# Kernel tuning notes

Hardware: AMD Instinct MI355X
Metric: run time of the kernel (lower is better)

Reference implementation:

```python
import jax, jax.numpy as jnp
import numpy as np

B, NAG = 8192, 16          # scenes, agents per scene
CIN, CH = 64, 128          # gnn_in_channels, gnn_out_channels
R2 = 8.0 * 8.0             # comm_range squared
BOX = 20.0                 # positions sampled uniformly in [0, BOX]^2


def _lin(k, fi, fo):
    k1, k2 = jax.random.split(k)
    s = 1.0 / np.sqrt(fi)
    W = jax.random.uniform(k1, (fi, fo), jnp.float32, -s, s)
    b = jax.random.uniform(k2, (fo,), jnp.float32, -s, s)
    return W, b


def setup_inputs() -> dict:
    key = jax.random.key(0)
    ks = jax.random.split(key, 10)
    x = jax.random.normal(ks[0], (B * NAG, CIN), jnp.float32)          # VAE mu per agent
    pos = jax.random.uniform(ks[1], (B, NAG, 2), jnp.float32) * BOX    # sensor xy positions
    W_rel1, b_rel1 = _lin(ks[2], CIN, CH)
    W_root1, _ = _lin(ks[3], CIN, CH)
    W_rel2, b_rel2 = _lin(ks[4], CH, CH)
    W_root2, _ = _lin(ks[5], CH, CH)
    Wh1, bh1 = _lin(ks[6], 2 * CH, 64)
    Wh2, bh2 = _lin(ks[7], 64, 32)
    Wh3, bh3 = _lin(ks[8], 32, 16)
    return dict(x=x, pos=pos, W_rel1=W_rel1, b_rel1=b_rel1, W_root1=W_root1,
                W_rel2=W_rel2, b_rel2=b_rel2, W_root2=W_root2,
                Wh1=Wh1, bh1=bh1, Wh2=Wh2, bh2=bh2, Wh3=Wh3, bh3=bh3)


def _graph_conv(h, adj, W_rel, b_rel, W_root):
    # PyG GraphConv (aggr='add'): out_i = W_rel @ sum_{j in N(i)} h_j + b_rel + W_root @ h_i
    nb = adj.shape[0]
    hb = h.reshape(nb, NAG, h.shape[-1])                 # [B, n, C]
    agg = jnp.einsum('bij,bjc->bic', adj, hb)            # neighbor sum within each scene
    return agg.reshape(h.shape[0], -1) @ W_rel + b_rel + h @ W_root


def reference(x, pos, W_rel1, b_rel1, W_root1, W_rel2, b_rel2, W_root2,
              Wh1, bh1, Wh2, bh2, Wh3, bh3):
    # radius_graph (batch-isolated, loop=False) as a per-scene dense mask
    diff = pos[:, :, None, :] - pos[:, None, :, :]       # [B, n, n, 2]
    d2 = jnp.sum(diff * diff, axis=-1)                   # [B, n, n]
    eye = jnp.eye(NAG, dtype=bool)
    adj = ((d2 <= R2) & ~eye).astype(x.dtype)            # [B, n, n]
    # Dropout(p=0.2) omitted (eval / deterministic reference).
    x1 = jax.nn.relu(_graph_conv(x, adj, W_rel1, b_rel1, W_root1))   # named 'x1' (inplace ReLU)
    x2 = jax.nn.relu(_graph_conv(x1, adj, W_rel2, b_rel2, W_root2))  # named 'x2' (inplace ReLU)
    h = jnp.concatenate([x1, x2], axis=-1)               # JumpingKnowledge('cat')
    h = jax.nn.relu(h @ Wh1 + bh1)
    h = jax.nn.relu(h @ Wh2 + bh2)
    out = h @ Wh3 + bh3                                  # [N, 16]
    return out.reshape(B, NAG, 16)
```

## Files before the change

kernel.cpp:

```cpp
#include <hip/hip_runtime.h>

#define NAG 16
#define SPB 4
#define NBLK 2048
#define R2f 64.0f

typedef unsigned short u16;
typedef __attribute__((ext_vector_type(8))) short short8;
typedef __attribute__((ext_vector_type(4))) float f32x4;

#define MFMA(a, b, c) __builtin_amdgcn_mfma_f32_16x16x32_bf16(a, b, c, 0, 0, 0)

#define OFF_B1 0
#define OFF_B2 16384
#define OFF_H1 49152
#define OFF_H2 65536
#define OFF_H3 67584
#define SWZ_UNITS 8512

__device__ __forceinline__ u16 f2b(float f) {
    unsigned u = __float_as_uint(f);
    unsigned r = u + 0x7FFFu + ((u >> 16) & 1u);
    return (u16)(r >> 16);
}
__device__ __forceinline__ unsigned rb(float f) {
    return (__float_as_uint(f) + 0x8000u) >> 16;
}
__device__ __forceinline__ unsigned pk2(float a, float b) {
    return ((__float_as_uint(a) + 0x8000u) >> 16) |
           ((__float_as_uint(b) + 0x8000u) & 0xFFFF0000u);
}

__global__ __launch_bounds__(256) void swizzle_w(
    const float* __restrict__ Wrel1, const float* __restrict__ Wroot1,
    const float* __restrict__ Wrel2, const float* __restrict__ Wroot2,
    const float* __restrict__ Wh1,  const float* __restrict__ Wh2,
    const float* __restrict__ Wh3,  u16* __restrict__ ws)
{
    const int u = blockIdx.x * 256 + threadIdx.x;
    if (u >= SWZ_UNITS) return;
    int v, T, N, ksplit;
    const float *W, *W2;
    u16* dst;
    if (u < 2048)      { v = u;        T = 8; N = 128; ksplit = 64;  W = Wroot1; W2 = Wrel1; dst = ws + OFF_B1 + v * 8; }
    else if (u < 6144) { v = u - 2048; T = 8; N = 128; ksplit = 128; W = Wroot2; W2 = Wrel2; dst = ws + OFF_B2 + v * 8; }
    else if (u < 8192) { v = u - 6144; T = 4; N = 64;  ksplit = 1 << 30; W = Wh1; W2 = Wh1; dst = ws + OFF_H1 + v * 8; }
    else if (u < 8448) { v = u - 8192; T = 2; N = 32;  ksplit = 1 << 30; W = Wh2; W2 = Wh2; dst = ws + OFF_H2 + v * 8; }
    else               { v = u - 8448; T = 1; N = 16;  ksplit = 1 << 30; W = Wh3; W2 = Wh3; dst = ws + OFF_H3 + v * 8; }
    const int lane = v & 63;
    const int t = (v >> 6) % T;
    const int s = (v >> 6) / T;
    const int n = t * 16 + (lane & 15);
    const int k0 = s * 32 + (lane >> 4) * 8;
    #pragma unroll
    for (int j = 0; j < 8; ++j) {
        const int k = k0 + j;
        const float val = (k < ksplit) ? W[k * N + n] : W2[(k - ksplit) * N + n];
        dst[j] = f2b(val);
    }
}

__device__ __forceinline__ short8 ldfrag(const u16* __restrict__ ws, int off,
                                         int T, int s, int tile, int lane) {
    return *(const short8*)(ws + off + (size_t)(((s * T + tile) * 64 + lane) * 8));
}

__device__ __forceinline__ short8 make_adjA(unsigned m, int q, int odd) {
    union { short8 v; unsigned u[4]; } r;
    const bool on = (q >> 1) == odd;
    const int base = (q & 1) * 8;
    #pragma unroll
    for (int jj = 0; jj < 4; ++jj) {
        const int k0 = base + 2 * jj;
        const unsigned lo = (on && ((m >> k0) & 1u)) ? 0x3F80u : 0u;
        const unsigned hi = (on && ((m >> (k0 + 1)) & 1u)) ? 0x3F80u : 0u;
        r.u[jj] = lo | (hi << 16);
    }
    return r.v;
}

__global__ __launch_bounds__(256) void gnn_fused5(
    const float* __restrict__ x, const float* __restrict__ pos,
    const float* __restrict__ brel1, const float* __restrict__ brel2,
    const float* __restrict__ bh1,  const float* __restrict__ bh2,
    const float* __restrict__ bh3,
    const u16* __restrict__ ws, float* __restrict__ out)
{
    __shared__ __align__(16) u16 pool[26624];
    __shared__ unsigned mask[64];
    u16* const xb  = pool;
    u16* const yT  = pool + 8704;
    u16* const x1b = pool + 17920;

    const int t = threadIdx.x;
    const int wv = t >> 6, lane = t & 63, ln = lane & 15, q = lane >> 4;
    const int c0 = 32 * wv;
    const int n0 = 2 * wv, n1 = 2 * wv + 1;
    const size_t sA = (size_t)blockIdx.x * SPB;

    {
        const int r = t >> 2, co = (t & 3) * 16;
        const float* src = x + (sA * 16 + r) * 64 + co;
        const float4 v0 = *(const float4*)(src);
        const float4 v1 = *(const float4*)(src + 4);
        const float4 v2 = *(const float4*)(src + 8);
        const float4 v3 = *(const float4*)(src + 12);
        uint4 ua, ub;
        ua.x = pk2(v0.x, v0.y); ua.y = pk2(v0.z, v0.w);
        ua.z = pk2(v1.x, v1.y); ua.w = pk2(v1.z, v1.w);
        ub.x = pk2(v2.x, v2.y); ub.y = pk2(v2.z, v2.w);
        ub.z = pk2(v3.x, v3.y); ub.w = pk2(v3.z, v3.w);
        *(uint4*)&xb[r * 136 + co]     = ua;
        *(uint4*)&xb[r * 136 + co + 8] = ub;
    }
    if (t < 64) {
        const int g = t >> 4, a = t & 15;
        const float* pp = pos + (sA + g) * (NAG * 2);
        const float ax = pp[2 * a], ay = pp[2 * a + 1];
        unsigned m = 0;
        for (int j = 0; j < NAG; ++j) {
            const float dx = ax - pp[2 * j], dy = ay - pp[2 * j + 1];
            if (dx * dx + dy * dy <= R2f && j != a) m |= (1u << j);
        }
        mask[g * 16 + a] = m;
    }
    __syncthreads();

    short8 adjA[4];
    #pragma unroll
    for (int g = 0; g < 4; ++g) adjA[g] = make_adjA(mask[g * 16 + ln], q, g & 1);

    {
        short8 Brl[2][2], Bro[2][2], Af[4][2];
        #pragma unroll
        for (int s = 0; s < 2; ++s) {
            Brl[s][0] = ldfrag(ws, OFF_B1, 8, s + 2, n0, lane);
            Brl[s][1] = ldfrag(ws, OFF_B1, 8, s + 2, n1, lane);
        }
        #pragma unroll
        for (int m = 0; m < 4; ++m) {
            Af[m][0] = *(const short8*)&xb[(m * 16 + ln) * 136 + q * 8];
            Af[m][1] = *(const short8*)&xb[(m * 16 + ln) * 136 + 32 + q * 8];
            f32x4 a0 = {0.f, 0.f, 0.f, 0.f}, a1 = a0;
            a0 = MFMA(Af[m][0], Brl[0][0], a0); a0 = MFMA(Af[m][1], Brl[1][0], a0);
            a1 = MFMA(Af[m][0], Brl[0][1], a1); a1 = MFMA(Af[m][1], Brl[1][1], a1);
            uint2 u0; u0.x = pk2(a0[0], a0[1]); u0.y = pk2(a0[2], a0[3]);
            uint2 u1; u1.x = pk2(a1[0], a1[1]); u1.y = pk2(a1[2], a1[3]);
            *(uint2*)&yT[(c0 + ln) * 72 + m * 16 + q * 4]      = u0;
            *(uint2*)&yT[(c0 + 16 + ln) * 72 + m * 16 + q * 4] = u1;
        }
        short8 By[2][2];
        #pragma unroll
        for (int w = 0; w < 2; ++w) {
            By[w][0] = *(const short8*)&yT[(c0 + ln) * 72 + w * 32 + q * 8];
            By[w][1] = *(const short8*)&yT[(c0 + 16 + ln) * 72 + w * 32 + q * 8];
        }
        #pragma unroll
        for (int s = 0; s < 2; ++s) {
            Bro[s][0] = ldfrag(ws, OFF_B1, 8, s, n0, lane);
            Bro[s][1] = ldfrag(ws, OFF_B1, 8, s, n1, lane);
        }
        const float b0 = brel1[c0 + ln], b1 = brel1[c0 + 16 + ln];
        #pragma unroll
        for (int g = 0; g < 4; ++g) {
            f32x4 a0 = {b0, b0, b0, b0}, a1 = {b1, b1, b1, b1};
            a0 = MFMA(Af[g][0], Bro[0][0], a0); a0 = MFMA(Af[g][1], Bro[1][0], a0);
            a1 = MFMA(Af[g][0], Bro[0][1], a1); a1 = MFMA(Af[g][1], Bro[1][1], a1);
            a0 = MFMA(adjA[g], By[g >> 1][0], a0);
            a1 = MFMA(adjA[g], By[g >> 1][1], a1);
            #pragma unroll
            for (int r = 0; r < 4; ++r) {
                const int row = g * 16 + q * 4 + r;
                x1b[row * 136 + c0 + ln]      = (u16)rb(fmaxf(a0[r], 0.f));
                x1b[row * 136 + c0 + 16 + ln] = (u16)rb(fmaxf(a1[r], 0.f));
            }
        }
    }
    __syncthreads();

    {
        short8 Brl[4][2];
        #pragma unroll
        for (int s = 0; s < 4; ++s) {
            Brl[s][0] = ldfrag(ws, OFF_B2, 8, s + 4, n0, lane);
            Brl[s][1] = ldfrag(ws, OFF_B2, 8, s + 4, n1, lane);
        }
        #pragma unroll
        for (int m = 0; m < 4; ++m) {
            f32x4 a0 = {0.f, 0.f, 0.f, 0.f}, a1 = a0;
            #pragma unroll
            for (int s = 0; s < 4; ++s) {
                const short8 A = *(const short8*)&x1b[(m * 16 + ln) * 136 + s * 32 + q * 8];
                a0 = MFMA(A, Brl[s][0], a0);
                a1 = MFMA(A, Brl[s][1], a1);
            }
            uint2 u0; u0.x = pk2(a0[0], a0[1]); u0.y = pk2(a0[2], a0[3]);
            uint2 u1; u1.x = pk2(a1[0], a1[1]); u1.y = pk2(a1[2], a1[3]);
            *(uint2*)&yT[(c0 + ln) * 72 + m * 16 + q * 4]      = u0;
            *(uint2*)&yT[(c0 + 16 + ln) * 72 + m * 16 + q * 4] = u1;
        }
        short8 By[2][2];
        #pragma unroll
        for (int w = 0; w < 2; ++w) {
            By[w][0] = *(const short8*)&yT[(c0 + ln) * 72 + w * 32 + q * 8];
            By[w][1] = *(const short8*)&yT[(c0 + 16 + ln) * 72 + w * 32 + q * 8];
        }
        short8 Bro[4][2];
        #pragma unroll
        for (int s = 0; s < 4; ++s) {
            Bro[s][0] = ldfrag(ws, OFF_B2, 8, s, n0, lane);
            Bro[s][1] = ldfrag(ws, OFF_B2, 8, s, n1, lane);
        }
        const float b0 = brel2[c0 + ln], b1 = brel2[c0 + 16 + ln];
        #pragma unroll
        for (int g = 0; g < 4; ++g) {
            f32x4 a0 = {b0, b0, b0, b0}, a1 = {b1, b1, b1, b1};
            #pragma unroll
            for (int s = 0; s < 4; ++s) {
                const short8 A = *(const short8*)&x1b[(g * 16 + ln) * 136 + s * 32 + q * 8];
                a0 = MFMA(A, Bro[s][0], a0);
                a1 = MFMA(A, Bro[s][1], a1);
            }
            a0 = MFMA(adjA[g], By[g >> 1][0], a0);
            a1 = MFMA(adjA[g], By[g >> 1][1], a1);
            #pragma unroll
            for (int r = 0; r < 4; ++r) {
                const int row = g * 16 + q * 4 + r;
                xb[row * 136 + c0 + ln]      = (u16)rb(fmaxf(a0[r], 0.f));
                xb[row * 136 + c0 + 16 + ln] = (u16)rb(fmaxf(a1[r], 0.f));
            }
        }
    }
    __syncthreads();

    {
        short8 Bf[8];
        #pragma unroll
        for (int s = 0; s < 8; ++s) Bf[s] = ldfrag(ws, OFF_H1, 4, s, wv, lane);
        const float b = bh1[wv * 16 + ln];
        #pragma unroll
        for (int m = 0; m < 4; ++m) {
            f32x4 a = {b, b, b, b}, c = {0.f, 0.f, 0.f, 0.f};
            #pragma unroll
            for (int s = 0; s < 4; ++s) {
                const short8 A1 = *(const short8*)&x1b[(m * 16 + ln) * 136 + s * 32 + q * 8];
                const short8 A2 = *(const short8*)&xb[(m * 16 + ln) * 136 + s * 32 + q * 8];
                a = MFMA(A1, Bf[s], a);
                c = MFMA(A2, Bf[s + 4], c);
            }
            #pragma unroll
            for (int r = 0; r < 4; ++r)
                yT[(m * 16 + q * 4 + r) * 72 + wv * 16 + ln] = (u16)rb(fmaxf(a[r] + c[r], 0.f));
        }
    }
    __syncthreads();

    {
        const u16* h1b = yT;
        u16* h2b = x1b;
        const short8 A0 = *(const short8*)&h1b[(wv * 16 + ln) * 72 + q * 8];
        const short8 A1 = *(const short8*)&h1b[(wv * 16 + ln) * 72 + 32 + q * 8];
        #pragma unroll
        for (int nt = 0; nt < 2; ++nt) {
            const short8 B0 = ldfrag(ws, OFF_H2, 2, 0, nt, lane);
            const short8 B1 = ldfrag(ws, OFF_H2, 2, 1, nt, lane);
            const float b = bh2[nt * 16 + ln];
            f32x4 a = {b, b, b, b};
            a = MFMA(A0, B0, a);
            a = MFMA(A1, B1, a);
            #pragma unroll
            for (int r = 0; r < 4; ++r)
                h2b[(wv * 16 + q * 4 + r) * 40 + nt * 16 + ln] = (u16)rb(fmaxf(a[r], 0.f));
        }
        const short8 A = *(const short8*)&h2b[(wv * 16 + ln) * 40 + q * 8];
        const short8 B = ldfrag(ws, OFF_H3, 1, 0, 0, lane);
        const float b = bh3[ln];
        f32x4 a = {b, b, b, b};
        a = MFMA(A, B, a);
        #pragma unroll
        for (int r = 0; r < 4; ++r)
            out[(sA * 16 + wv * 16 + q * 4 + r) * 16 + ln] = a[r];
    }
}

extern "C" void kernel_launch(void* const* d_in, const int* in_sizes, int n_in,
                              void* d_out, int out_size, void* d_ws, size_t ws_size,
                              hipStream_t stream) {
    const float* x      = (const float*)d_in[0];
    const float* pos    = (const float*)d_in[1];
    const float* Wrel1  = (const float*)d_in[2];
    const float* brel1  = (const float*)d_in[3];
    const float* Wroot1 = (const float*)d_in[4];
    const float* Wrel2  = (const float*)d_in[5];
    const float* brel2  = (const float*)d_in[6];
    const float* Wroot2 = (const float*)d_in[7];
    const float* Wh1    = (const float*)d_in[8];
    const float* bh1    = (const float*)d_in[9];
    const float* Wh2    = (const float*)d_in[10];
    const float* bh2    = (const float*)d_in[11];
    const float* Wh3    = (const float*)d_in[12];
    const float* bh3    = (const float*)d_in[13];
    u16* ws = (u16*)d_ws;

    swizzle_w<<<(SWZ_UNITS + 255) / 256, 256, 0, stream>>>(
        Wrel1, Wroot1, Wrel2, Wroot2, Wh1, Wh2, Wh3, ws);
    gnn_fused5<<<NBLK, 256, 0, stream>>>(
        x, pos, brel1, brel2, bh1, bh2, bh3, ws, (float*)d_out);
}
```

Measured before the change: 125.0 us.

## Double block to 512 threads, one 16-column tile per wave

Each block now has eight waves instead of four. In the GraphConv layers each wave owns one 16-column output tile rather than two. The first head layer splits work by column tile and row half, and the final head layers run on four waves only. The aim is more wavefronts and more latency hiding per CU with fewer registers per wave. The cost is that each A-fragment read from LDS is now repeated across more waves, and the idle waves in the tail stage waste slots.

```diff
diff --git a/kernel.cpp b/kernel.cpp
--- a/kernel.cpp
+++ b/kernel.cpp
@@ -3,6 +3,7 @@
 #define NAG 16
 #define SPB 4
 #define NBLK 2048
+#define TPB 512
 #define R2f 64.0f
 
 typedef unsigned short u16;
@@ -79,7 +80,7 @@
     return r.v;
 }
 
-__global__ __launch_bounds__(256) void gnn_fused5(
+__global__ __launch_bounds__(TPB) void gnn_fused6(
     const float* __restrict__ x, const float* __restrict__ pos,
     const float* __restrict__ brel1, const float* __restrict__ brel2,
     const float* __restrict__ bh1,  const float* __restrict__ bh2,
@@ -94,24 +95,18 @@
 
     const int t = threadIdx.x;
     const int wv = t >> 6, lane = t & 63, ln = lane & 15, q = lane >> 4;
-    const int c0 = 32 * wv;
-    const int n0 = 2 * wv, n1 = 2 * wv + 1;
+    const int c0 = 16 * wv;
     const size_t sA = (size_t)blockIdx.x * SPB;
 
     {
-        const int r = t >> 2, co = (t & 3) * 16;
+        const int r = t >> 3, co = (t & 7) * 8;
         const float* src = x + (sA * 16 + r) * 64 + co;
         const float4 v0 = *(const float4*)(src);
         const float4 v1 = *(const float4*)(src + 4);
-        const float4 v2 = *(const float4*)(src + 8);
-        const float4 v3 = *(const float4*)(src + 12);
-        uint4 ua, ub;
+        uint4 ua;
         ua.x = pk2(v0.x, v0.y); ua.y = pk2(v0.z, v0.w);
         ua.z = pk2(v1.x, v1.y); ua.w = pk2(v1.z, v1.w);
-        ub.x = pk2(v2.x, v2.y); ub.y = pk2(v2.z, v2.w);
-        ub.z = pk2(v3.x, v3.y); ub.w = pk2(v3.z, v3.w);
-        *(uint4*)&xb[r * 136 + co]     = ua;
-        *(uint4*)&xb[r * 136 + co + 8] = ub;
+        *(uint4*)&xb[r * 136 + co] = ua;
     }
     if (t < 64) {
         const int g = t >> 4, a = t & 15;
@@ -131,115 +126,88 @@
     for (int g = 0; g < 4; ++g) adjA[g] = make_adjA(mask[g * 16 + ln], q, g & 1);
 
     {
-        short8 Brl[2][2], Bro[2][2], Af[4][2];
+        short8 Brl[2], Bro[2], Af[4][2];
         #pragma unroll
         for (int s = 0; s < 2; ++s) {
-            Brl[s][0] = ldfrag(ws, OFF_B1, 8, s + 2, n0, lane);
-            Brl[s][1] = ldfrag(ws, OFF_B1, 8, s + 2, n1, lane);
+            Brl[s] = ldfrag(ws, OFF_B1, 8, s + 2, wv, lane);
+            Bro[s] = ldfrag(ws, OFF_B1, 8, s, wv, lane);
         }
         #pragma unroll
         for (int m = 0; m < 4; ++m) {
             Af[m][0] = *(const short8*)&xb[(m * 16 + ln) * 136 + q * 8];
             Af[m][1] = *(const short8*)&xb[(m * 16 + ln) * 136 + 32 + q * 8];
-            f32x4 a0 = {0.f, 0.f, 0.f, 0.f}, a1 = a0;
-            a0 = MFMA(Af[m][0], Brl[0][0], a0); a0 = MFMA(Af[m][1], Brl[1][0], a0);
-            a1 = MFMA(Af[m][0], Brl[0][1], a1); a1 = MFMA(Af[m][1], Brl[1][1], a1);
+            f32x4 a0 = {0.f, 0.f, 0.f, 0.f};
+            a0 = MFMA(Af[m][0], Brl[0], a0);
+            a0 = MFMA(Af[m][1], Brl[1], a0);
             uint2 u0; u0.x = pk2(a0[0], a0[1]); u0.y = pk2(a0[2], a0[3]);
-            uint2 u1; u1.x = pk2(a1[0], a1[1]); u1.y = pk2(a1[2], a1[3]);
-            *(uint2*)&yT[(c0 + ln) * 72 + m * 16 + q * 4]      = u0;
-            *(uint2*)&yT[(c0 + 16 + ln) * 72 + m * 16 + q * 4] = u1;
-        }
-        short8 By[2][2];
-        #pragma unroll
-        for (int w = 0; w < 2; ++w) {
-            By[w][0] = *(const short8*)&yT[(c0 + ln) * 72 + w * 32 + q * 8];
-            By[w][1] = *(const short8*)&yT[(c0 + 16 + ln) * 72 + w * 32 + q * 8];
-        }
-        #pragma unroll
-        for (int s = 0; s < 2; ++s) {
-            Bro[s][0] = ldfrag(ws, OFF_B1, 8, s, n0, lane);
-            Bro[s][1] = ldfrag(ws, OFF_B1, 8, s, n1, lane);
-        }
-        const float b0 = brel1[c0 + ln], b1 = brel1[c0 + 16 + ln];
+            *(uint2*)&yT[(c0 + ln) * 72 + m * 16 + q * 4] = u0;
+        }
+        short8 By[2];
+        #pragma unroll
+        for (int w = 0; w < 2; ++w)
+            By[w] = *(const short8*)&yT[(c0 + ln) * 72 + w * 32 + q * 8];
+        const float b0 = brel1[c0 + ln];
         #pragma unroll
         for (int g = 0; g < 4; ++g) {
-            f32x4 a0 = {b0, b0, b0, b0}, a1 = {b1, b1, b1, b1};
-            a0 = MFMA(Af[g][0], Bro[0][0], a0); a0 = MFMA(Af[g][1], Bro[1][0], a0);
-            a1 = MFMA(Af[g][0], Bro[0][1], a1); a1 = MFMA(Af[g][1], Bro[1][1], a1);
-            a0 = MFMA(adjA[g], By[g >> 1][0], a0);
-            a1 = MFMA(adjA[g], By[g >> 1][1], a1);
-            #pragma unroll
-            for (int r = 0; r < 4; ++r) {
-                const int row = g * 16 + q * 4 + r;
-                x1b[row * 136 + c0 + ln]      = (u16)rb(fmaxf(a0[r], 0.f));
-                x1b[row * 136 + c0 + 16 + ln] = (u16)rb(fmaxf(a1[r], 0.f));
-            }
-        }
-    }
-    __syncthreads();
-
-    {
-        short8 Brl[4][2];
-        #pragma unroll
-        for (int s = 0; s < 4; ++s) {
-            Brl[s][0] = ldfrag(ws, OFF_B2, 8, s + 4, n0, lane);
-            Brl[s][1] = ldfrag(ws, OFF_B2, 8, s + 4, n1, lane);
-        }
+            f32x4 a0 = {b0, b0, b0, b0};
+            a0 = MFMA(Af[g][0], Bro[0], a0);
+            a0 = MFMA(Af[g][1], Bro[1], a0);
+            a0 = MFMA(adjA[g], By[g >> 1], a0);
+            #pragma unroll
+            for (int r = 0; r < 4; ++r)
+                x1b[(g * 16 + q * 4 + r) * 136 + c0 + ln] = (u16)rb(fmaxf(a0[r], 0.f));
+        }
+    }
+    __syncthreads();
+
+    {
+        short8 Brl[4];
+        #pragma unroll
+        for (int s = 0; s < 4; ++s) Brl[s] = ldfrag(ws, OFF_B2, 8, s + 4, wv, lane);
         #pragma unroll
         for (int m = 0; m < 4; ++m) {
-            f32x4 a0 = {0.f, 0.f, 0.f, 0.f}, a1 = a0;
+            f32x4 a0 = {0.f, 0.f, 0.f, 0.f};
             #pragma unroll
             for (int s = 0; s < 4; ++s) {
                 const short8 A = *(const short8*)&x1b[(m * 16 + ln) * 136 + s * 32 + q * 8];
-                a0 = MFMA(A, Brl[s][0], a0);
-                a1 = MFMA(A, Brl[s][1], a1);
+                a0 = MFMA(A, Brl[s], a0);
             }
             uint2 u0; u0.x = pk2(a0[0], a0[1]); u0.y = pk2(a0[2], a0[3]);
-            uint2 u1; u1.x = pk2(a1[0], a1[1]); u1.y = pk2(a1[2], a1[3]);
-            *(uint2*)&yT[(c0 + ln) * 72 + m * 16 + q * 4]      = u0;
-            *(uint2*)&yT[(c0 + 16 + ln) * 72 + m * 16 + q * 4] = u1;
-        }
-        short8 By[2][2];
-        #pragma unroll
-        for (int w = 0; w < 2; ++w) {
-            By[w][0] = *(const short8*)&yT[(c0 + ln) * 72 + w * 32 + q * 8];
-            By[w][1] = *(const short8*)&yT[(c0 + 16 + ln) * 72 + w * 32 + q * 8];
-        }
-        short8 Bro[4][2];
-        #pragma unroll
-        for (int s = 0; s < 4; ++s) {
-            Bro[s][0] = ldfrag(ws, OFF_B2, 8, s, n0, lane);
-            Bro[s][1] = ldfrag(ws, OFF_B2, 8, s, n1, lane);
-        }
-        const float b0 = brel2[c0 + ln], b1 = brel2[c0 + 16 + ln];
+            *(uint2*)&yT[(c0 + ln) * 72 + m * 16 + q * 4] = u0;
+        }
+        short8 By[2];
+        #pragma unroll
+        for (int w = 0; w < 2; ++w)
+            By[w] = *(const short8*)&yT[(c0 + ln) * 72 + w * 32 + q * 8];
+        short8 Bro[4];
+        #pragma unroll
+        for (int s = 0; s < 4; ++s) Bro[s] = ldfrag(ws, OFF_B2, 8, s, wv, lane);
+        const float b0 = brel2[c0 + ln];
         #pragma unroll
         for (int g = 0; g < 4; ++g) {
-            f32x4 a0 = {b0, b0, b0, b0}, a1 = {b1, b1, b1, b1};
+            f32x4 a0 = {b0, b0, b0, b0};
             #pragma unroll
             for (int s = 0; s < 4; ++s) {
                 const short8 A = *(const short8*)&x1b[(g * 16 + ln) * 136 + s * 32 + q * 8];
-                a0 = MFMA(A, Bro[s][0], a0);
-                a1 = MFMA(A, Bro[s][1], a1);
+                a0 = MFMA(A, Bro[s], a0);
             }
-            a0 = MFMA(adjA[g], By[g >> 1][0], a0);
-            a1 = MFMA(adjA[g], By[g >> 1][1], a1);
-            #pragma unroll
-            for (int r = 0; r < 4; ++r) {
-                const int row = g * 16 + q * 4 + r;
-                xb[row * 136 + c0 + ln]      = (u16)rb(fmaxf(a0[r], 0.f));
-                xb[row * 136 + c0 + 16 + ln] = (u16)rb(fmaxf(a1[r], 0.f));
-            }
-        }
-    }
-    __syncthreads();
-
-    {
+            a0 = MFMA(adjA[g], By[g >> 1], a0);
+            #pragma unroll
+            for (int r = 0; r < 4; ++r)
+                xb[(g * 16 + q * 4 + r) * 136 + c0 + ln] = (u16)rb(fmaxf(a0[r], 0.f));
+        }
+    }
+    __syncthreads();
+
+    {
+        const int nt = wv & 3, mh = wv >> 2;
         short8 Bf[8];
         #pragma unroll
-        for (int s = 0; s < 8; ++s) Bf[s] = ldfrag(ws, OFF_H1, 4, s, wv, lane);
-        const float b = bh1[wv * 16 + ln];
-        #pragma unroll
-        for (int m = 0; m < 4; ++m) {
+        for (int s = 0; s < 8; ++s) Bf[s] = ldfrag(ws, OFF_H1, 4, s, nt, lane);
+        const float b = bh1[nt * 16 + ln];
+        #pragma unroll
+        for (int mi = 0; mi < 2; ++mi) {
+            const int m = 2 * mh + mi;
             f32x4 a = {b, b, b, b}, c = {0.f, 0.f, 0.f, 0.f};
             #pragma unroll
             for (int s = 0; s < 4; ++s) {
@@ -250,12 +218,12 @@
             }
             #pragma unroll
             for (int r = 0; r < 4; ++r)
-                yT[(m * 16 + q * 4 + r) * 72 + wv * 16 + ln] = (u16)rb(fmaxf(a[r] + c[r], 0.f));
-        }
-    }
-    __syncthreads();
-
-    {
+                yT[(m * 16 + q * 4 + r) * 72 + nt * 16 + ln] = (u16)rb(fmaxf(a[r] + c[r], 0.f));
+        }
+    }
+    __syncthreads();
+
+    if (wv < 4) {
         const u16* h1b = yT;
         u16* h2b = x1b;
         const short8 A0 = *(const short8*)&h1b[(wv * 16 + ln) * 72 + q * 8];
@@ -304,6 +272,6 @@
 
     swizzle_w<<<(SWZ_UNITS + 255) / 256, 256, 0, stream>>>(
         Wrel1, Wroot1, Wrel2, Wroot2, Wh1, Wh2, Wh3, ws);
-    gnn_fused5<<<NBLK, 256, 0, stream>>>(
+    gnn_fused6<<<NBLK, TPB, 0, stream>>>(
         x, pos, brel1, brel2, bh1, bh2, bh3, ws, (float*)d_out);
 }
```

New measurement: 126.6 us. No clear change (+1.3%).
